# Kernel tuning notes

Hardware: AMD Instinct MI355X
Metric: run time of the kernel (lower is better)

Reference implementation:

```python
import jax, jax.numpy as jnp
import numpy as np

B, L, N, D = 4096, 50, 50, 128
STD = 0.1


def setup_inputs() -> dict:
    key = jax.random.key(0)
    ks = jax.random.split(key, 6)
    seq_idx = jax.random.randint(ks[0], (B, L), 0, N, dtype=jnp.int32)
    mask = jnp.ones((B, L), dtype=jnp.int32)
    node_vectors = jax.random.normal(ks[1], (B, N, D), dtype=jnp.float32)
    u = lambda k, shp: jax.random.uniform(k, shp, jnp.float32, -STD, STD)
    return {
        "sequence_of_indexes": seq_idx,
        "mask": mask,
        "node_vectors": node_vectors,
        "batch_size": B,
        "W_last": u(ks[2], (D, D)),      # dense_last_item kernel (no bias)
        "W_seq": u(ks[3], (D, D)),       # dense_sequence_items kernel
        "b_seq": jnp.zeros((D,), jnp.float32),  # dense_sequence_items bias
        "W_alpha": u(ks[4], (D, 1)),     # dense_alpha kernel (no bias)
    }


def reference(sequence_of_indexes, mask, node_vectors, batch_size,
              W_last, W_seq, b_seq, W_alpha):
    maskf = mask.astype(jnp.float32)                          # [B, L]
    seq_len = jnp.sum(maskf, axis=1).astype(jnp.int32)        # [B]
    rows = jnp.arange(batch_size)
    # last item index per session, then gather its node vector
    last_idx = sequence_of_indexes[rows, seq_len - 1]         # [B]
    v_n = node_vectors[rows, last_idx]                        # [B, D]
    # per-batch embedding lookup: node_vectors[b, seq_idx[b]]
    v_i = jnp.take_along_axis(node_vectors, sequence_of_indexes[..., None], axis=1)  # [B, L, D]
    vn_proj = (v_n @ W_last)[:, None, :]                      # [B, 1, D]
    vi_proj = v_i @ W_seq + b_seq                             # [B, L, D]
    alpha = jax.nn.sigmoid(vn_proj + vi_proj) @ W_alpha       # [B, L, 1]
    alpha = alpha * maskf[..., None]
    session_graph = jnp.sum(alpha * v_i, axis=1)              # [B, D]
    return v_n, session_graph
```

## Files before the change

### kernel.cpp

```cpp
#include <hip/hip_runtime.h>
#include <math.h>

#define BB 4096
#define LL 50
#define NN 50
#define DD 128
#define STR 136

typedef short bf16x8 __attribute__((ext_vector_type(8)));
typedef float f32x4  __attribute__((ext_vector_type(4)));

static __device__ inline unsigned short f32_to_bf16_rne(float f) {
    unsigned int u = __float_as_uint(f);
    u += 0x7FFFu + ((u >> 16) & 1u);
    return (unsigned short)(u >> 16);
}
static __device__ inline float bf16_to_f32(unsigned short h) {
    return __uint_as_float(((unsigned int)h) << 16);
}

__global__ void prep_w(const float* __restrict__ W_seq,
                       const float* __restrict__ W_last,
                       unsigned short* __restrict__ ws)
{
    int t = blockIdx.x * blockDim.x + threadIdx.x;
    int lane = t & 63;
    int nt   = (t >> 6) & 7;
    int kk   = t >> 9;
    const float* W = (kk < 4) ? W_seq : W_last;
    int kb = (kk & 3) * 32 + (lane >> 4) * 8;
    int n  = nt * 16 + (lane & 15);
    unsigned short* dst = ws + (size_t)t * 8;
    #pragma unroll
    for (int j = 0; j < 8; ++j)
        dst[j] = f32_to_bf16_rne(W[(kb + j) * DD + n]);
}

__global__ __launch_bounds__(256, 3) void sess_attn(
    const int*   __restrict__ seq_idx,
    const int*   __restrict__ mask,
    const float* __restrict__ nodes,
    const float* __restrict__ b_seq,
    const float* __restrict__ W_alpha,
    const unsigned short* __restrict__ wfrag,
    float*       __restrict__ out)
{
    const int b    = blockIdx.x;
    const int tid  = threadIdx.x;
    const int lane = tid & 63;
    const int wave = tid >> 6;
    const int col  = lane & 15;
    const int quad = lane >> 4;

    __shared__ __align__(16) unsigned short s_nbf[64][STR];
    __shared__ float s_alpha[64];
    __shared__ float s_cntf[64];
    __shared__ int   s_last;

    const float4* nb4 = (const float4*)(nodes + (size_t)b * (NN * DD));
    float4 v[7];
    #pragma unroll
    for (int j = 0; j < 6; ++j) v[j] = nb4[tid + j * 256];
    if (tid < 64) v[6] = nb4[tid + 1536];

    const bf16x8* wsf = (const bf16x8*)wfrag;
    bf16x8 bfS[8], bfL[8];
    #pragma unroll
    for (int kk = 0; kk < 4; ++kk)
        #pragma unroll
        for (int j = 0; j < 2; ++j) {
            bfS[kk * 2 + j] = wsf[(size_t)(((kk    ) * 8 + wave * 2 + j) * 64 + lane)];
            bfL[kk * 2 + j] = wsf[(size_t)(((kk + 4) * 8 + wave * 2 + j) * 64 + lane)];
        }

    int pm = 0, pi = 0;
    if (tid < 64) {
        pm = (tid < LL) ? mask[b * LL + tid]    : 0;
        pi = (tid < LL) ? seq_idx[b * LL + tid] : 0;
    }

    float bb_r[2], wa_r[2];
    #pragma unroll
    for (int j = 0; j < 2; ++j) {
        int n = (wave * 2 + j) * 16 + col;
        bb_r[j] = b_seq[n];
        wa_r[j] = W_alpha[n];
    }

    if (tid < 64) { s_alpha[tid] = 0.f; s_cntf[tid] = 0.f; }

    #pragma unroll
    for (int j = 0; j < 6; ++j) {
        int idx = tid + j * 256;
        int r = idx >> 5, c = (idx & 31) * 4;
        ushort4 h;
        h.x = f32_to_bf16_rne(v[j].x);
        h.y = f32_to_bf16_rne(v[j].y);
        h.z = f32_to_bf16_rne(v[j].z);
        h.w = f32_to_bf16_rne(v[j].w);
        *(ushort4*)&s_nbf[r][c] = h;
    }
    if (tid < 64) {
        int idx = tid + 1536;
        int r = idx >> 5, c = (idx & 31) * 4;
        ushort4 h;
        h.x = f32_to_bf16_rne(v[6].x);
        h.y = f32_to_bf16_rne(v[6].y);
        h.z = f32_to_bf16_rne(v[6].z);
        h.w = f32_to_bf16_rne(v[6].w);
        *(ushort4*)&s_nbf[r][c] = h;
    }

    if (tid < 64) {
        int mm = pm;
        mm += __shfl_xor(mm, 1);  mm += __shfl_xor(mm, 2);
        mm += __shfl_xor(mm, 4);  mm += __shfl_xor(mm, 8);
        mm += __shfl_xor(mm, 16); mm += __shfl_xor(mm, 32);
        int j = mm - 1;
        if (j < 0) j += LL;
        int li = __shfl(pi, j);
        if (tid == 0) s_last = li;
        if (tid < LL && pm) atomicAdd(&s_cntf[pi], (float)pm);
    }
    __syncthreads();

    const int last = s_last;

    if (tid < DD)
        out[(size_t)b * DD + tid] = nodes[(size_t)b * (NN * DD) + last * DD + tid];

    f32x4 acc[4][2];
    #pragma unroll
    for (int m = 0; m < 4; ++m)
        #pragma unroll
        for (int j = 0; j < 2; ++j)
            acc[m][j] = (f32x4){0.f, 0.f, 0.f, 0.f};
    f32x4 accV[2];
    #pragma unroll
    for (int j = 0; j < 2; ++j)
        accV[j] = (f32x4){bb_r[j], bb_r[j], bb_r[j], bb_r[j]};

    #pragma unroll
    for (int kk = 0; kk < 4; ++kk) {
        bf16x8 a[4];
        #pragma unroll
        for (int m = 0; m < 4; ++m)
            a[m] = *(const bf16x8*)&s_nbf[m * 16 + col][kk * 32 + quad * 8];
        bf16x8 av = *(const bf16x8*)&s_nbf[last][kk * 32 + quad * 8];
        #pragma unroll
        for (int j = 0; j < 2; ++j) {
            #pragma unroll
            for (int m = 0; m < 4; ++m)
                acc[m][j] = __builtin_amdgcn_mfma_f32_16x16x32_bf16(
                    a[m], bfS[kk * 2 + j], acc[m][j], 0, 0, 0);
            accV[j] = __builtin_amdgcn_mfma_f32_16x16x32_bf16(
                av, bfL[kk * 2 + j], accV[j], 0, 0, 0);
        }
    }

    #pragma unroll
    for (int m = 0; m < 4; ++m) {
        float pr[4] = {0.f, 0.f, 0.f, 0.f};
        #pragma unroll
        for (int j = 0; j < 2; ++j) {
            float wa = wa_r[j];
            #pragma unroll
            for (int r = 0; r < 4; ++r) {
                float x = acc[m][j][r] + accV[j][r];
                float sig = 1.f / (1.f + __expf(-x));
                pr[r] = fmaf(sig, wa, pr[r]);
            }
        }
        #pragma unroll
        for (int r = 0; r < 4; ++r) {
            float vv = pr[r];
            vv += __shfl_xor(vv, 1);
            vv += __shfl_xor(vv, 2);
            vv += __shfl_xor(vv, 4);
            vv += __shfl_xor(vv, 8);
            int row = m * 16 + quad * 4 + r;
            if (col == 0 && row < NN) atomicAdd(&s_alpha[row], vv);
        }
    }
    __syncthreads();

    if (tid < DD) {
        float acc2 = 0.f;
        #pragma unroll 10
        for (int n = 0; n < NN; ++n)
            acc2 = fmaf(s_cntf[n] * s_alpha[n], bf16_to_f32(s_nbf[n][tid]), acc2);
        out[(size_t)BB * DD + (size_t)b * DD + tid] = acc2;
    }
}

extern "C" void kernel_launch(void* const* d_in, const int* in_sizes, int n_in,
                              void* d_out, int out_size, void* d_ws, size_t ws_size,
                              hipStream_t stream) {
    const int*   seq     = (const int*)  d_in[0];
    const int*   mask    = (const int*)  d_in[1];
    const float* nodes   = (const float*)d_in[2];
    const float* W_last  = (const float*)d_in[4];
    const float* W_seq   = (const float*)d_in[5];
    const float* b_seq   = (const float*)d_in[6];
    const float* W_alpha = (const float*)d_in[7];
    float*       out     = (float*)      d_out;

    unsigned short* wsf = (unsigned short*)d_ws;

    prep_w<<<16, 256, 0, stream>>>(W_seq, W_last, wsf);
    sess_attn<<<BB, 256, 0, stream>>>(seq, mask, nodes, b_seq, W_alpha, wsf, out);
}
```

Measured before the change: 178.6 us.

## Process each session with a single wave, removing block barriers and atomics

Restructures the attention kernel from a 4-wave block to one 64-lane wave per batch element, with each lane loading 25 float4 of node vectors and looping over all eight output-column tiles. Weight fragments are streamed from global memory per tile instead of being held in registers, and the alpha reduction writes directly instead of using shared atomics. This aims to remove __syncthreads and atomic overhead. In exchange it adds more work and register pressure per wave and may reduce latency hiding.

```diff
diff --git a/kernel.cpp b/kernel.cpp
--- a/kernel.cpp
+++ b/kernel.cpp
@@ -36,7 +36,7 @@
         dst[j] = f32_to_bf16_rne(W[(kb + j) * DD + n]);
 }
 
-__global__ __launch_bounds__(256, 3) void sess_attn(
+__global__ __launch_bounds__(64, 3) void sess_attn(
     const int*   __restrict__ seq_idx,
     const int*   __restrict__ mask,
     const float* __restrict__ nodes,
@@ -46,151 +46,143 @@
     float*       __restrict__ out)
 {
     const int b    = blockIdx.x;
-    const int tid  = threadIdx.x;
-    const int lane = tid & 63;
-    const int wave = tid >> 6;
+    const int lane = threadIdx.x;
     const int col  = lane & 15;
     const int quad = lane >> 4;
 
-    __shared__ __align__(16) unsigned short s_nbf[64][STR];
-    __shared__ float s_alpha[64];
-    __shared__ float s_cntf[64];
-    __shared__ int   s_last;
+    __shared__ __align__(16) unsigned short s_t[NN * STR];
+    __shared__ float s_alpha[NN];
+    __shared__ float s_cnt[NN];
 
     const float4* nb4 = (const float4*)(nodes + (size_t)b * (NN * DD));
-    float4 v[7];
-    #pragma unroll
-    for (int j = 0; j < 6; ++j) v[j] = nb4[tid + j * 256];
-    if (tid < 64) v[6] = nb4[tid + 1536];
-
-    const bf16x8* wsf = (const bf16x8*)wfrag;
-    bf16x8 bfS[8], bfL[8];
-    #pragma unroll
-    for (int kk = 0; kk < 4; ++kk)
-        #pragma unroll
-        for (int j = 0; j < 2; ++j) {
-            bfS[kk * 2 + j] = wsf[(size_t)(((kk    ) * 8 + wave * 2 + j) * 64 + lane)];
-            bfL[kk * 2 + j] = wsf[(size_t)(((kk + 4) * 8 + wave * 2 + j) * 64 + lane)];
-        }
+    float4 v[25];
+    #pragma unroll
+    for (int i = 0; i < 25; ++i) v[i] = nb4[lane + i * 64];
 
     int pm = 0, pi = 0;
-    if (tid < 64) {
-        pm = (tid < LL) ? mask[b * LL + tid]    : 0;
-        pi = (tid < LL) ? seq_idx[b * LL + tid] : 0;
-    }
-
-    float bb_r[2], wa_r[2];
-    #pragma unroll
-    for (int j = 0; j < 2; ++j) {
-        int n = (wave * 2 + j) * 16 + col;
-        bb_r[j] = b_seq[n];
-        wa_r[j] = W_alpha[n];
-    }
-
-    if (tid < 64) { s_alpha[tid] = 0.f; s_cntf[tid] = 0.f; }
-
-    #pragma unroll
-    for (int j = 0; j < 6; ++j) {
-        int idx = tid + j * 256;
+    if (lane < LL) {
+        pm = mask[b * LL + lane];
+        pi = seq_idx[b * LL + lane];
+    }
+
+    float bb[8], wa[8];
+    #pragma unroll
+    for (int j = 0; j < 8; ++j) {
+        int n = j * 16 + col;
+        bb[j] = b_seq[n];
+        wa[j] = W_alpha[n];
+    }
+
+    if (lane < NN) s_cnt[lane] = 0.f;
+
+    #pragma unroll
+    for (int i = 0; i < 25; ++i) {
+        int idx = lane + i * 64;
         int r = idx >> 5, c = (idx & 31) * 4;
         ushort4 h;
-        h.x = f32_to_bf16_rne(v[j].x);
-        h.y = f32_to_bf16_rne(v[j].y);
-        h.z = f32_to_bf16_rne(v[j].z);
-        h.w = f32_to_bf16_rne(v[j].w);
-        *(ushort4*)&s_nbf[r][c] = h;
-    }
-    if (tid < 64) {
-        int idx = tid + 1536;
-        int r = idx >> 5, c = (idx & 31) * 4;
-        ushort4 h;
-        h.x = f32_to_bf16_rne(v[6].x);
-        h.y = f32_to_bf16_rne(v[6].y);
-        h.z = f32_to_bf16_rne(v[6].z);
-        h.w = f32_to_bf16_rne(v[6].w);
-        *(ushort4*)&s_nbf[r][c] = h;
-    }
-
-    if (tid < 64) {
-        int mm = pm;
-        mm += __shfl_xor(mm, 1);  mm += __shfl_xor(mm, 2);
-        mm += __shfl_xor(mm, 4);  mm += __shfl_xor(mm, 8);
-        mm += __shfl_xor(mm, 16); mm += __shfl_xor(mm, 32);
-        int j = mm - 1;
-        if (j < 0) j += LL;
-        int li = __shfl(pi, j);
-        if (tid == 0) s_last = li;
-        if (tid < LL && pm) atomicAdd(&s_cntf[pi], (float)pm);
-    }
-    __syncthreads();
-
-    const int last = s_last;
-
-    if (tid < DD)
-        out[(size_t)b * DD + tid] = nodes[(size_t)b * (NN * DD) + last * DD + tid];
-
-    f32x4 acc[4][2];
+        h.x = f32_to_bf16_rne(v[i].x);
+        h.y = f32_to_bf16_rne(v[i].y);
+        h.z = f32_to_bf16_rne(v[i].z);
+        h.w = f32_to_bf16_rne(v[i].w);
+        *(ushort4*)&s_t[r * STR + c] = h;
+    }
+
+    int mm = pm;
+    mm += __shfl_xor(mm, 1);  mm += __shfl_xor(mm, 2);
+    mm += __shfl_xor(mm, 4);  mm += __shfl_xor(mm, 8);
+    mm += __shfl_xor(mm, 16); mm += __shfl_xor(mm, 32);
+    int jl = mm - 1;
+    if (jl < 0) jl += LL;
+    const int last = __shfl(pi, jl);
+    if (lane < LL && pm) atomicAdd(&s_cnt[pi], (float)pm);
+
+    {
+        const float2* vn2 = (const float2*)(nodes + (size_t)b * (NN * DD) + (size_t)last * DD);
+        ((float2*)(out + (size_t)b * DD))[lane] = vn2[lane];
+    }
+
+    const bf16x8* wsf = (const bf16x8*)wfrag;
+
+    bf16x8 av[4];
+    #pragma unroll
+    for (int kk = 0; kk < 4; ++kk)
+        av[kk] = *(const bf16x8*)&s_t[last * STR + kk * 32 + quad * 8];
+    float c8[8];
+    #pragma unroll
+    for (int j = 0; j < 8; ++j) {
+        f32x4 aV = (f32x4){bb[j], bb[j], bb[j], bb[j]};
+        #pragma unroll
+        for (int kk = 0; kk < 4; ++kk)
+            aV = __builtin_amdgcn_mfma_f32_16x16x32_bf16(
+                av[kk], wsf[(size_t)(((kk + 4) * 8 + j) * 64 + lane)], aV, 0, 0, 0);
+        c8[j] = aV[0];
+    }
+
+    float pr[4][4];
     #pragma unroll
     for (int m = 0; m < 4; ++m)
         #pragma unroll
-        for (int j = 0; j < 2; ++j)
-            acc[m][j] = (f32x4){0.f, 0.f, 0.f, 0.f};
-    f32x4 accV[2];
-    #pragma unroll
-    for (int j = 0; j < 2; ++j)
-        accV[j] = (f32x4){bb_r[j], bb_r[j], bb_r[j], bb_r[j]};
-
-    #pragma unroll
-    for (int kk = 0; kk < 4; ++kk) {
-        bf16x8 a[4];
+        for (int r = 0; r < 4; ++r) pr[m][r] = 0.f;
+
+    const int ar0 = col, ar1 = 16 + col, ar2 = 32 + col;
+    const int ar3 = (48 + col > NN - 1) ? (NN - 1) : (48 + col);
+
+    #pragma unroll
+    for (int j = 0; j < 8; ++j) {
+        f32x4 acc[4];
+        #pragma unroll
+        for (int m = 0; m < 4; ++m) acc[m] = (f32x4){0.f, 0.f, 0.f, 0.f};
+        #pragma unroll
+        for (int kk = 0; kk < 4; ++kk) {
+            bf16x8 bs = wsf[(size_t)((kk * 8 + j) * 64 + lane)];
+            int co = kk * 32 + quad * 8;
+            bf16x8 a0 = *(const bf16x8*)&s_t[ar0 * STR + co];
+            bf16x8 a1 = *(const bf16x8*)&s_t[ar1 * STR + co];
+            bf16x8 a2 = *(const bf16x8*)&s_t[ar2 * STR + co];
+            bf16x8 a3 = *(const bf16x8*)&s_t[ar3 * STR + co];
+            acc[0] = __builtin_amdgcn_mfma_f32_16x16x32_bf16(a0, bs, acc[0], 0, 0, 0);
+            acc[1] = __builtin_amdgcn_mfma_f32_16x16x32_bf16(a1, bs, acc[1], 0, 0, 0);
+            acc[2] = __builtin_amdgcn_mfma_f32_16x16x32_bf16(a2, bs, acc[2], 0, 0, 0);
+            acc[3] = __builtin_amdgcn_mfma_f32_16x16x32_bf16(a3, bs, acc[3], 0, 0, 0);
+        }
+        float cj = c8[j], waj = wa[j];
         #pragma unroll
         for (int m = 0; m < 4; ++m)
-            a[m] = *(const bf16x8*)&s_nbf[m * 16 + col][kk * 32 + quad * 8];
-        bf16x8 av = *(const bf16x8*)&s_nbf[last][kk * 32 + quad * 8];
-        #pragma unroll
-        for (int j = 0; j < 2; ++j) {
-            #pragma unroll
-            for (int m = 0; m < 4; ++m)
-                acc[m][j] = __builtin_amdgcn_mfma_f32_16x16x32_bf16(
-                    a[m], bfS[kk * 2 + j], acc[m][j], 0, 0, 0);
-            accV[j] = __builtin_amdgcn_mfma_f32_16x16x32_bf16(
-                av, bfL[kk * 2 + j], accV[j], 0, 0, 0);
-        }
-    }
-
-    #pragma unroll
-    for (int m = 0; m < 4; ++m) {
-        float pr[4] = {0.f, 0.f, 0.f, 0.f};
-        #pragma unroll
-        for (int j = 0; j < 2; ++j) {
-            float wa = wa_r[j];
             #pragma unroll
             for (int r = 0; r < 4; ++r) {
-                float x = acc[m][j][r] + accV[j][r];
+                float x = acc[m][r] + cj;
                 float sig = 1.f / (1.f + __expf(-x));
-                pr[r] = fmaf(sig, wa, pr[r]);
+                pr[m][r] = fmaf(sig, waj, pr[m][r]);
             }
-        }
+    }
+
+    #pragma unroll
+    for (int m = 0; m < 4; ++m) {
         #pragma unroll
         for (int r = 0; r < 4; ++r) {
-            float vv = pr[r];
+            float vv = pr[m][r];
             vv += __shfl_xor(vv, 1);
             vv += __shfl_xor(vv, 2);
             vv += __shfl_xor(vv, 4);
             vv += __shfl_xor(vv, 8);
             int row = m * 16 + quad * 4 + r;
-            if (col == 0 && row < NN) atomicAdd(&s_alpha[row], vv);
+            if (col == 0 && row < NN) s_alpha[row] = vv;
         }
     }
-    __syncthreads();
-
-    if (tid < DD) {
-        float acc2 = 0.f;
-        #pragma unroll 10
-        for (int n = 0; n < NN; ++n)
-            acc2 = fmaf(s_cntf[n] * s_alpha[n], bf16_to_f32(s_nbf[n][tid]), acc2);
-        out[(size_t)BB * DD + (size_t)b * DD + tid] = acc2;
-    }
+
+    if (lane < NN) s_alpha[lane] *= s_cnt[lane];
+
+    float a0 = 0.f, a1 = 0.f;
+    const int d0 = lane * 2;
+    #pragma unroll 10
+    for (int n = 0; n < NN; ++n) {
+        float wn = s_alpha[n];
+        unsigned int tv = *(const unsigned int*)&s_t[n * STR + d0];
+        a0 = fmaf(wn, bf16_to_f32((unsigned short)(tv & 0xFFFFu)), a0);
+        a1 = fmaf(wn, bf16_to_f32((unsigned short)(tv >> 16)), a1);
+    }
+    float2 o; o.x = a0; o.y = a1;
+    ((float2*)(out + (size_t)BB * DD + (size_t)b * DD))[lane] = o;
 }
 
 extern "C" void kernel_launch(void* const* d_in, const int* in_sizes, int n_in,
@@ -208,5 +200,5 @@
     unsigned short* wsf = (unsigned short*)d_ws;
 
     prep_w<<<16, 256, 0, stream>>>(W_seq, W_last, wsf);
-    sess_attn<<<BB, 256, 0, stream>>>(seq, mask, nodes, b_seq, W_alpha, wsf, out);
-}
+    sess_attn<<<BB, 64, 0, stream>>>(seq, mask, nodes, b_seq, W_alpha, wsf, out);
+}
```

New measurement: 232.5 us. +30.2%, slower.

## Load node tile straight into LDS as fp32 with XOR swizzle, convert at use

Applied to the files above, without the earlier changes.

Replaces the register-staged global load plus bf16 conversion with direct global-to-LDS async loads (global_load_lds) into an XOR-swizzled fp32 tile. Conversion to bf16 moves to the MFMA operand fetch, and the final weighted sum now reads full fp32 node values. The W_last fragments are loaded inside the k-loop instead of being held in registers, and launch bounds rise to 4 blocks per CU. This trades double the LDS footprint (25.6KB vs ~17KB) and repeated per-use conversions for removing the register round-trip and lowering register pressure.

```diff
diff --git a/kernel.cpp b/kernel.cpp
--- a/kernel.cpp
+++ b/kernel.cpp
@@ -5,7 +5,6 @@
 #define LL 50
 #define NN 50
 #define DD 128
-#define STR 136
 
 typedef short bf16x8 __attribute__((ext_vector_type(8)));
 typedef float f32x4  __attribute__((ext_vector_type(4)));
@@ -15,8 +14,18 @@
     u += 0x7FFFu + ((u >> 16) & 1u);
     return (unsigned short)(u >> 16);
 }
-static __device__ inline float bf16_to_f32(unsigned short h) {
-    return __uint_as_float(((unsigned int)h) << 16);
+
+static __device__ inline bf16x8 pack8(float4 lo, float4 hi) {
+    bf16x8 r;
+    r[0] = (short)f32_to_bf16_rne(lo.x);
+    r[1] = (short)f32_to_bf16_rne(lo.y);
+    r[2] = (short)f32_to_bf16_rne(lo.z);
+    r[3] = (short)f32_to_bf16_rne(lo.w);
+    r[4] = (short)f32_to_bf16_rne(hi.x);
+    r[5] = (short)f32_to_bf16_rne(hi.y);
+    r[6] = (short)f32_to_bf16_rne(hi.z);
+    r[7] = (short)f32_to_bf16_rne(hi.w);
+    return r;
 }
 
 __global__ void prep_w(const float* __restrict__ W_seq,
@@ -36,7 +45,7 @@
         dst[j] = f32_to_bf16_rne(W[(kb + j) * DD + n]);
 }
 
-__global__ __launch_bounds__(256, 3) void sess_attn(
+__global__ __launch_bounds__(256, 4) void sess_attn(
     const int*   __restrict__ seq_idx,
     const int*   __restrict__ mask,
     const float* __restrict__ nodes,
@@ -52,26 +61,12 @@
     const int col  = lane & 15;
     const int quad = lane >> 4;
 
-    __shared__ __align__(16) unsigned short s_nbf[64][STR];
+    __shared__ __align__(16) float s_f[NN * DD];
     __shared__ float s_alpha[64];
-    __shared__ float s_cntf[64];
+    __shared__ float s_cnt[64];
     __shared__ int   s_last;
 
-    const float4* nb4 = (const float4*)(nodes + (size_t)b * (NN * DD));
-    float4 v[7];
-    #pragma unroll
-    for (int j = 0; j < 6; ++j) v[j] = nb4[tid + j * 256];
-    if (tid < 64) v[6] = nb4[tid + 1536];
-
-    const bf16x8* wsf = (const bf16x8*)wfrag;
-    bf16x8 bfS[8], bfL[8];
-    #pragma unroll
-    for (int kk = 0; kk < 4; ++kk)
-        #pragma unroll
-        for (int j = 0; j < 2; ++j) {
-            bfS[kk * 2 + j] = wsf[(size_t)(((kk    ) * 8 + wave * 2 + j) * 64 + lane)];
-            bfL[kk * 2 + j] = wsf[(size_t)(((kk + 4) * 8 + wave * 2 + j) * 64 + lane)];
-        }
+    const float* nb = nodes + (size_t)b * (NN * DD);
 
     int pm = 0, pi = 0;
     if (tid < 64) {
@@ -79,82 +74,101 @@
         pi = (tid < LL) ? seq_idx[b * LL + tid] : 0;
     }
 
+    #pragma unroll
+    for (int i = 0; i < 6; ++i) {
+        int p  = i * 256 + tid;
+        int r  = p >> 5;
+        int Bk = p & 31;
+        const float* src = nb + r * DD + ((Bk ^ (r & 7)) << 2);
+        __builtin_amdgcn_global_load_lds(
+            (const __attribute__((address_space(1))) unsigned int*)src,
+            (__attribute__((address_space(3))) unsigned int*)(&s_f[(i * 256 + wave * 64) * 4]),
+            16, 0, 0);
+    }
+    if (tid < 64) {
+        int p  = 1536 + tid;
+        int r  = p >> 5, Bk = p & 31;
+        const float* src = nb + r * DD + ((Bk ^ (r & 7)) << 2);
+        __builtin_amdgcn_global_load_lds(
+            (const __attribute__((address_space(1))) unsigned int*)src,
+            (__attribute__((address_space(3))) unsigned int*)(&s_f[1536 * 4]),
+            16, 0, 0);
+    }
+
+    const bf16x8* wsf = (const bf16x8*)wfrag;
+    bf16x8 bfS[8];
+    #pragma unroll
+    for (int kk = 0; kk < 4; ++kk)
+        #pragma unroll
+        for (int j2 = 0; j2 < 2; ++j2)
+            bfS[kk * 2 + j2] = wsf[(size_t)((kk * 8 + wave * 2 + j2) * 64 + lane)];
+
     float bb_r[2], wa_r[2];
     #pragma unroll
-    for (int j = 0; j < 2; ++j) {
-        int n = (wave * 2 + j) * 16 + col;
-        bb_r[j] = b_seq[n];
-        wa_r[j] = W_alpha[n];
-    }
-
-    if (tid < 64) { s_alpha[tid] = 0.f; s_cntf[tid] = 0.f; }
-
-    #pragma unroll
-    for (int j = 0; j < 6; ++j) {
-        int idx = tid + j * 256;
-        int r = idx >> 5, c = (idx & 31) * 4;
-        ushort4 h;
-        h.x = f32_to_bf16_rne(v[j].x);
-        h.y = f32_to_bf16_rne(v[j].y);
-        h.z = f32_to_bf16_rne(v[j].z);
-        h.w = f32_to_bf16_rne(v[j].w);
-        *(ushort4*)&s_nbf[r][c] = h;
-    }
+    for (int j2 = 0; j2 < 2; ++j2) {
+        int n = (wave * 2 + j2) * 16 + col;
+        bb_r[j2] = b_seq[n];
+        wa_r[j2] = W_alpha[n];
+    }
+
     if (tid < 64) {
-        int idx = tid + 1536;
-        int r = idx >> 5, c = (idx & 31) * 4;
-        ushort4 h;
-        h.x = f32_to_bf16_rne(v[6].x);
-        h.y = f32_to_bf16_rne(v[6].y);
-        h.z = f32_to_bf16_rne(v[6].z);
-        h.w = f32_to_bf16_rne(v[6].w);
-        *(ushort4*)&s_nbf[r][c] = h;
-    }
-
-    if (tid < 64) {
+        s_alpha[tid] = 0.f;
+        s_cnt[tid]   = 0.f;
         int mm = pm;
         mm += __shfl_xor(mm, 1);  mm += __shfl_xor(mm, 2);
         mm += __shfl_xor(mm, 4);  mm += __shfl_xor(mm, 8);
         mm += __shfl_xor(mm, 16); mm += __shfl_xor(mm, 32);
-        int j = mm - 1;
-        if (j < 0) j += LL;
-        int li = __shfl(pi, j);
+        int jl = mm - 1;
+        if (jl < 0) jl += LL;
+        int li = __shfl(pi, jl);
         if (tid == 0) s_last = li;
-        if (tid < LL && pm) atomicAdd(&s_cntf[pi], (float)pm);
-    }
+        if (tid < LL && pm) atomicAdd(&s_cnt[pi], (float)pm);
+    }
+
     __syncthreads();
 
     const int last = s_last;
+    const int sL   = last & 7;
 
     if (tid < DD)
-        out[(size_t)b * DD + tid] = nodes[(size_t)b * (NN * DD) + last * DD + tid];
+        out[(size_t)b * DD + tid] =
+            s_f[last * DD + (((tid >> 2) ^ sL) << 2) + (tid & 3)];
 
     f32x4 acc[4][2];
     #pragma unroll
     for (int m = 0; m < 4; ++m)
         #pragma unroll
-        for (int j = 0; j < 2; ++j)
-            acc[m][j] = (f32x4){0.f, 0.f, 0.f, 0.f};
+        for (int j2 = 0; j2 < 2; ++j2)
+            acc[m][j2] = (f32x4){0.f, 0.f, 0.f, 0.f};
     f32x4 accV[2];
     #pragma unroll
-    for (int j = 0; j < 2; ++j)
-        accV[j] = (f32x4){bb_r[j], bb_r[j], bb_r[j], bb_r[j]};
+    for (int j2 = 0; j2 < 2; ++j2)
+        accV[j2] = (f32x4){bb_r[j2], bb_r[j2], bb_r[j2], bb_r[j2]};
 
     #pragma unroll
     for (int kk = 0; kk < 4; ++kk) {
+        const int B1 = kk * 8 + quad * 2;
         bf16x8 a[4];
         #pragma unroll
-        for (int m = 0; m < 4; ++m)
-            a[m] = *(const bf16x8*)&s_nbf[m * 16 + col][kk * 32 + quad * 8];
-        bf16x8 av = *(const bf16x8*)&s_nbf[last][kk * 32 + quad * 8];
-        #pragma unroll
-        for (int j = 0; j < 2; ++j) {
-            #pragma unroll
-            for (int m = 0; m < 4; ++m)
-                acc[m][j] = __builtin_amdgcn_mfma_f32_16x16x32_bf16(
-                    a[m], bfS[kk * 2 + j], acc[m][j], 0, 0, 0);
-            accV[j] = __builtin_amdgcn_mfma_f32_16x16x32_bf16(
-                av, bfL[kk * 2 + j], accV[j], 0, 0, 0);
+        for (int m = 0; m < 4; ++m) {
+            int r = m * 16 + col;
+            if (r > NN - 1) r = NN - 1;
+            int s = r & 7;
+            float4 lo = *(const float4*)&s_f[r * DD + ((B1 ^ s) << 2)];
+            float4 hi = *(const float4*)&s_f[r * DD + (((B1 + 1) ^ s) << 2)];
+            a[m] = pack8(lo, hi);
+        }
+        float4 vlo = *(const float4*)&s_f[last * DD + ((B1 ^ sL) << 2)];
+        float4 vhi = *(const float4*)&s_f[last * DD + (((B1 + 1) ^ sL) << 2)];
+        bf16x8 av = pack8(vlo, vhi);
+        #pragma unroll
+        for (int j2 = 0; j2 < 2; ++j2) {
+            bf16x8 bl = wsf[(size_t)(((kk + 4) * 8 + wave * 2 + j2) * 64 + lane)];
+            acc[0][j2] = __builtin_amdgcn_mfma_f32_16x16x32_bf16(a[0], bfS[kk * 2 + j2], acc[0][j2], 0, 0, 0);
+            acc[1][j2] = __builtin_amdgcn_mfma_f32_16x16x32_bf16(a[1], bfS[kk * 2 + j2], acc[1][j2], 0, 0, 0);
+            acc[2][j2] = __builtin_amdgcn_mfma_f32_16x16x32_bf16(a[2], bfS[kk * 2 + j2], acc[2][j2], 0, 0, 0);
+            acc[3][j2] = __builtin_amdgcn_mfma_f32_16x16x32_bf16(a[3], bfS[kk * 2 + j2], acc[3][j2], 0, 0, 0);
+            accV[j2]   = __builtin_amdgcn_mfma_f32_16x16x32_bf16(av,   bl,              accV[j2],   0, 0, 0);
         }
     }
 
@@ -162,13 +176,13 @@
     for (int m = 0; m < 4; ++m) {
         float pr[4] = {0.f, 0.f, 0.f, 0.f};
         #pragma unroll
-        for (int j = 0; j < 2; ++j) {
-            float wa = wa_r[j];
+        for (int j2 = 0; j2 < 2; ++j2) {
+            float waj = wa_r[j2];
             #pragma unroll
             for (int r = 0; r < 4; ++r) {
-                float x = acc[m][j][r] + accV[j][r];
+                float x = acc[m][j2][r] + accV[j2][r];
                 float sig = 1.f / (1.f + __expf(-x));
-                pr[r] = fmaf(sig, wa, pr[r]);
+                pr[r] = fmaf(sig, waj, pr[r]);
             }
         }
         #pragma unroll
@@ -185,10 +199,12 @@
     __syncthreads();
 
     if (tid < DD) {
+        const int Bd = tid >> 2, od = tid & 3;
         float acc2 = 0.f;
         #pragma unroll 10
         for (int n = 0; n < NN; ++n)
-            acc2 = fmaf(s_cntf[n] * s_alpha[n], bf16_to_f32(s_nbf[n][tid]), acc2);
+            acc2 = fmaf(s_cnt[n] * s_alpha[n],
+                        s_f[n * DD + ((Bd ^ (n & 7)) << 2) + od], acc2);
         out[(size_t)BB * DD + (size_t)b * DD + tid] = acc2;
     }
 }
```

New measurement: 191.3 us. +7.1%, slower.

## Use 512-thread blocks with one output column tile per wave

Applied to the files above, without the earlier changes.

Doubles the block to 8 waves so each wave owns one 16-column tile and folds the last-item projection into the same accumulator through extra MFMAs, replacing the split accV path. Weight fragments are now loaded inside the k-loop instead of preloaded, which cuts register pressure so the kernel can target 8 blocks per CU. The shared tile shrinks to 50 rows, and the fourth row block is clamped. The final reduction uses two accumulators. The risk is redundant MFMAs on the broadcast last vector and more global loads of the weight fragments.

```diff
diff --git a/kernel.cpp b/kernel.cpp
--- a/kernel.cpp
+++ b/kernel.cpp
@@ -36,7 +36,7 @@
         dst[j] = f32_to_bf16_rne(W[(kb + j) * DD + n]);
 }
 
-__global__ __launch_bounds__(256, 3) void sess_attn(
+__global__ __launch_bounds__(512, 8) void sess_attn(
     const int*   __restrict__ seq_idx,
     const int*   __restrict__ mask,
     const float* __restrict__ nodes,
@@ -52,26 +52,10 @@
     const int col  = lane & 15;
     const int quad = lane >> 4;
 
-    __shared__ __align__(16) unsigned short s_nbf[64][STR];
+    __shared__ __align__(16) unsigned short s_nbf[NN * STR];
     __shared__ float s_alpha[64];
-    __shared__ float s_cntf[64];
+    __shared__ float s_cnt[64];
     __shared__ int   s_last;
-
-    const float4* nb4 = (const float4*)(nodes + (size_t)b * (NN * DD));
-    float4 v[7];
-    #pragma unroll
-    for (int j = 0; j < 6; ++j) v[j] = nb4[tid + j * 256];
-    if (tid < 64) v[6] = nb4[tid + 1536];
-
-    const bf16x8* wsf = (const bf16x8*)wfrag;
-    bf16x8 bfS[8], bfL[8];
-    #pragma unroll
-    for (int kk = 0; kk < 4; ++kk)
-        #pragma unroll
-        for (int j = 0; j < 2; ++j) {
-            bfS[kk * 2 + j] = wsf[(size_t)(((kk    ) * 8 + wave * 2 + j) * 64 + lane)];
-            bfL[kk * 2 + j] = wsf[(size_t)(((kk + 4) * 8 + wave * 2 + j) * 64 + lane)];
-        }
 
     int pm = 0, pi = 0;
     if (tid < 64) {
@@ -79,36 +63,40 @@
         pi = (tid < LL) ? seq_idx[b * LL + tid] : 0;
     }
 
-    float bb_r[2], wa_r[2];
-    #pragma unroll
-    for (int j = 0; j < 2; ++j) {
-        int n = (wave * 2 + j) * 16 + col;
-        bb_r[j] = b_seq[n];
-        wa_r[j] = W_alpha[n];
-    }
-
-    if (tid < 64) { s_alpha[tid] = 0.f; s_cntf[tid] = 0.f; }
-
-    #pragma unroll
-    for (int j = 0; j < 6; ++j) {
-        int idx = tid + j * 256;
-        int r = idx >> 5, c = (idx & 31) * 4;
+    const float4* nb4 = (const float4*)(nodes + (size_t)b * (NN * DD));
+    float4 v0 = nb4[tid];
+    float4 v1 = nb4[tid + 512];
+    float4 v2 = nb4[tid + 1024];
+    float4 v3;
+    if (tid < 64) v3 = nb4[tid + 1536];
+
+    const int ncol = wave * 16 + col;
+    const float bb = b_seq[ncol];
+    const float wa = W_alpha[ncol];
+
+    if (tid < 64) { s_alpha[tid] = 0.f; s_cnt[tid] = 0.f; }
+
+    {
         ushort4 h;
-        h.x = f32_to_bf16_rne(v[j].x);
-        h.y = f32_to_bf16_rne(v[j].y);
-        h.z = f32_to_bf16_rne(v[j].z);
-        h.w = f32_to_bf16_rne(v[j].w);
-        *(ushort4*)&s_nbf[r][c] = h;
-    }
-    if (tid < 64) {
-        int idx = tid + 1536;
-        int r = idx >> 5, c = (idx & 31) * 4;
-        ushort4 h;
-        h.x = f32_to_bf16_rne(v[6].x);
-        h.y = f32_to_bf16_rne(v[6].y);
-        h.z = f32_to_bf16_rne(v[6].z);
-        h.w = f32_to_bf16_rne(v[6].w);
-        *(ushort4*)&s_nbf[r][c] = h;
+        int idx, r, c;
+        idx = tid;            r = idx >> 5; c = (idx & 31) * 4;
+        h.x = f32_to_bf16_rne(v0.x); h.y = f32_to_bf16_rne(v0.y);
+        h.z = f32_to_bf16_rne(v0.z); h.w = f32_to_bf16_rne(v0.w);
+        *(ushort4*)&s_nbf[r * STR + c] = h;
+        idx = tid + 512;      r = idx >> 5; c = (idx & 31) * 4;
+        h.x = f32_to_bf16_rne(v1.x); h.y = f32_to_bf16_rne(v1.y);
+        h.z = f32_to_bf16_rne(v1.z); h.w = f32_to_bf16_rne(v1.w);
+        *(ushort4*)&s_nbf[r * STR + c] = h;
+        idx = tid + 1024;     r = idx >> 5; c = (idx & 31) * 4;
+        h.x = f32_to_bf16_rne(v2.x); h.y = f32_to_bf16_rne(v2.y);
+        h.z = f32_to_bf16_rne(v2.z); h.w = f32_to_bf16_rne(v2.w);
+        *(ushort4*)&s_nbf[r * STR + c] = h;
+        if (tid < 64) {
+            idx = tid + 1536; r = idx >> 5; c = (idx & 31) * 4;
+            h.x = f32_to_bf16_rne(v3.x); h.y = f32_to_bf16_rne(v3.y);
+            h.z = f32_to_bf16_rne(v3.z); h.w = f32_to_bf16_rne(v3.w);
+            *(ushort4*)&s_nbf[r * STR + c] = h;
+        }
     }
 
     if (tid < 64) {
@@ -116,12 +104,13 @@
         mm += __shfl_xor(mm, 1);  mm += __shfl_xor(mm, 2);
         mm += __shfl_xor(mm, 4);  mm += __shfl_xor(mm, 8);
         mm += __shfl_xor(mm, 16); mm += __shfl_xor(mm, 32);
-        int j = mm - 1;
-        if (j < 0) j += LL;
-        int li = __shfl(pi, j);
+        int jl = mm - 1;
+        if (jl < 0) jl += LL;
+        int li = __shfl(pi, jl);
         if (tid == 0) s_last = li;
-        if (tid < LL && pm) atomicAdd(&s_cntf[pi], (float)pm);
-    }
+        if (tid < LL && pm) atomicAdd(&s_cnt[pi], (float)pm);
+    }
+
     __syncthreads();
 
     const int last = s_last;
@@ -129,47 +118,47 @@
     if (tid < DD)
         out[(size_t)b * DD + tid] = nodes[(size_t)b * (NN * DD) + last * DD + tid];
 
-    f32x4 acc[4][2];
+    f32x4 acc[4];
     #pragma unroll
     for (int m = 0; m < 4; ++m)
+        acc[m] = (f32x4){bb, bb, bb, bb};
+
+    const bf16x8* wsf = (const bf16x8*)wfrag;
+
+    #pragma unroll
+    for (int kk = 0; kk < 8; ++kk) {
+        const int co = (kk & 3) * 32 + quad * 8;
+        bf16x8 bfr = wsf[(size_t)((kk * 8 + wave) * 64 + lane)];
+        if (kk < 4) {
+            bf16x8 a0, a1, a2, a3;
+            {
+                int r0 = col, r1 = 16 + col, r2 = 32 + col;
+                int r3 = (48 + col > NN - 1) ? (NN - 1) : (48 + col);
+                a0 = *(const bf16x8*)&s_nbf[r0 * STR + co];
+                a1 = *(const bf16x8*)&s_nbf[r1 * STR + co];
+                a2 = *(const bf16x8*)&s_nbf[r2 * STR + co];
+                a3 = *(const bf16x8*)&s_nbf[r3 * STR + co];
+            }
+            acc[0] = __builtin_amdgcn_mfma_f32_16x16x32_bf16(a0, bfr, acc[0], 0, 0, 0);
+            acc[1] = __builtin_amdgcn_mfma_f32_16x16x32_bf16(a1, bfr, acc[1], 0, 0, 0);
+            acc[2] = __builtin_amdgcn_mfma_f32_16x16x32_bf16(a2, bfr, acc[2], 0, 0, 0);
+            acc[3] = __builtin_amdgcn_mfma_f32_16x16x32_bf16(a3, bfr, acc[3], 0, 0, 0);
+        } else {
+            bf16x8 av = *(const bf16x8*)&s_nbf[last * STR + co];
+            acc[0] = __builtin_amdgcn_mfma_f32_16x16x32_bf16(av, bfr, acc[0], 0, 0, 0);
+            acc[1] = __builtin_amdgcn_mfma_f32_16x16x32_bf16(av, bfr, acc[1], 0, 0, 0);
+            acc[2] = __builtin_amdgcn_mfma_f32_16x16x32_bf16(av, bfr, acc[2], 0, 0, 0);
+            acc[3] = __builtin_amdgcn_mfma_f32_16x16x32_bf16(av, bfr, acc[3], 0, 0, 0);
+        }
+    }
+
+    #pragma unroll
+    for (int m = 0; m < 4; ++m) {
+        float pr[4];
         #pragma unroll
-        for (int j = 0; j < 2; ++j)
-            acc[m][j] = (f32x4){0.f, 0.f, 0.f, 0.f};
-    f32x4 accV[2];
-    #pragma unroll
-    for (int j = 0; j < 2; ++j)
-        accV[j] = (f32x4){bb_r[j], bb_r[j], bb_r[j], bb_r[j]};
-
-    #pragma unroll
-    for (int kk = 0; kk < 4; ++kk) {
-        bf16x8 a[4];
-        #pragma unroll
-        for (int m = 0; m < 4; ++m)
-            a[m] = *(const bf16x8*)&s_nbf[m * 16 + col][kk * 32 + quad * 8];
-        bf16x8 av = *(const bf16x8*)&s_nbf[last][kk * 32 + quad * 8];
-        #pragma unroll
-        for (int j = 0; j < 2; ++j) {
-            #pragma unroll
-            for (int m = 0; m < 4; ++m)
-                acc[m][j] = __builtin_amdgcn_mfma_f32_16x16x32_bf16(
-                    a[m], bfS[kk * 2 + j], acc[m][j], 0, 0, 0);
-            accV[j] = __builtin_amdgcn_mfma_f32_16x16x32_bf16(
-                av, bfL[kk * 2 + j], accV[j], 0, 0, 0);
-        }
-    }
-
-    #pragma unroll
-    for (int m = 0; m < 4; ++m) {
-        float pr[4] = {0.f, 0.f, 0.f, 0.f};
-        #pragma unroll
-        for (int j = 0; j < 2; ++j) {
-            float wa = wa_r[j];
-            #pragma unroll
-            for (int r = 0; r < 4; ++r) {
-                float x = acc[m][j][r] + accV[j][r];
-                float sig = 1.f / (1.f + __expf(-x));
-                pr[r] = fmaf(sig, wa, pr[r]);
-            }
+        for (int r = 0; r < 4; ++r) {
+            float x = acc[m][r];
+            pr[r] = wa / (1.f + __expf(-x));
         }
         #pragma unroll
         for (int r = 0; r < 4; ++r) {
@@ -185,11 +174,15 @@
     __syncthreads();
 
     if (tid < DD) {
-        float acc2 = 0.f;
-        #pragma unroll 10
-        for (int n = 0; n < NN; ++n)
-            acc2 = fmaf(s_cntf[n] * s_alpha[n], bf16_to_f32(s_nbf[n][tid]), acc2);
-        out[(size_t)BB * DD + (size_t)b * DD + tid] = acc2;
+        float accA = 0.f, accB = 0.f;
+        #pragma unroll 5
+        for (int n = 0; n < NN; n += 2) {
+            float wA = s_cnt[n]     * s_alpha[n];
+            float wB = s_cnt[n + 1] * s_alpha[n + 1];
+            accA = fmaf(wA, bf16_to_f32(s_nbf[n * STR + tid]), accA);
+            accB = fmaf(wB, bf16_to_f32(s_nbf[(n + 1) * STR + tid]), accB);
+        }
+        out[(size_t)BB * DD + (size_t)b * DD + tid] = accA + accB;
     }
 }
 
@@ -208,5 +201,5 @@
     unsigned short* wsf = (unsigned short*)d_ws;
 
     prep_w<<<16, 256, 0, stream>>>(W_seq, W_last, wsf);
-    sess_attn<<<BB, 256, 0, stream>>>(seq, mask, nodes, b_seq, W_alpha, wsf, out);
-}
+    sess_attn<<<BB, 512, 0, stream>>>(seq, mask, nodes, b_seq, W_alpha, wsf, out);
+}
```

After: 187.5 us. 5.0% more time.
